# Performance work log

Hardware: AMD Instinct MI355X
Metric: run time of the kernel (lower is better)

The kernel has to match this reference:

```python
import jax, jax.numpy as jnp
import numpy as np
import math

N_HEAD = 16
N_KV_HEAD = 4
HEAD_DIM = 128  # n_embed // n_head


def apply_rope(x, omega, offset=0):
    # x: (B, T, H, D); omega: (D//2,) Llama-style inverse frequencies
    T = x.shape[1]
    d2 = x.shape[-1] // 2
    pos = (jnp.arange(T) + offset).astype(x.dtype)
    ang = pos[:, None] * omega[None, :]              # (T, d2)
    cos = jnp.cos(ang)[None, :, None, :]
    sin = jnp.sin(ang)[None, :, None, :]
    x1, x2 = x[..., :d2], x[..., d2:]
    return jnp.concatenate([x1 * cos - x2 * sin, x1 * sin + x2 * cos], axis=-1)


def setup_inputs() -> dict:
    key = jax.random.key(0)
    k1, k2, k3, k4 = jax.random.split(key, 4)
    B, T, C = 2, 2048, 2048
    std = 0.02
    x = jax.random.normal(k1, (B, T, C), dtype=jnp.float32)
    wq = jax.random.normal(k2, (C, C), dtype=jnp.float32) * std
    wkv = jax.random.normal(k3, (C, 2 * N_KV_HEAD * HEAD_DIM), dtype=jnp.float32) * std
    wproj = jax.random.normal(k4, (C, C), dtype=jnp.float32) * std * (2 * 24) ** (-0.5)
    # Llama RoPE frequencies: 1 / 10000^(2i/D)
    omega = (1.0 / (10000.0 ** (jnp.arange(0, HEAD_DIM, 2, dtype=jnp.float32) / HEAD_DIM)))
    return {"x": x, "wq": wq, "wkv": wkv, "wproj": wproj, "omega": omega}


def reference(x, wq, wkv, wproj, omega):
    B, T, C = x.shape
    H, KH, D = N_HEAD, N_KV_HEAD, HEAD_DIM
    G = H // KH  # query heads per kv head

    q = (x @ wq).reshape(B, T, H, D)
    kv = x @ wkv
    k, v = jnp.split(kv, 2, axis=-1)

    q = apply_rope(q, omega, offset=0)
    k = apply_rope(k.reshape(B, T, KH, D), omega, offset=0)
    v = v.reshape(B, T, KH, D)

    # GQA causal attention (no KV expansion: group query heads per kv head)
    qr = q.reshape(B, T, KH, G, D)
    scores = jnp.einsum('bqkgd,bskd->bkgqs', qr, k) / math.sqrt(D)
    causal = jnp.tril(jnp.ones((T, T), dtype=bool))
    scores = jnp.where(causal[None, None, None, :, :], scores, -jnp.inf)
    att = jax.nn.softmax(scores, axis=-1)
    y = jnp.einsum('bkgqs,bskd->bqkgd', att, v).reshape(B, T, C)
    return y @ wproj
```

## Files before the change

kernel.cpp:

```cpp
#include <hip/hip_runtime.h>
#include <hip/hip_bf16.h>

#define B_ 2
#define T_ 2048
#define C_ 2048
#define H_ 16
#define KH_ 4
#define D_ 128

typedef unsigned short ushort_t;
typedef __attribute__((ext_vector_type(8))) short short8;
typedef __attribute__((ext_vector_type(4))) float f32x4;

#define RSQRT_D 0.08838834764831845f
#define L2E 1.4426950408889634f
#define QSCALE (0.08838834764831845f * 1.4426950408889634f)

__device__ __forceinline__ ushort_t f2b(float f) {
  union { float f; unsigned u; } v; v.f = f;
  unsigned r = v.u + 0x7fffu + ((v.u >> 16) & 1u);
  return (ushort_t)(r >> 16);
}
__device__ __forceinline__ float b2f(ushort_t u) {
  union { unsigned u; float f; } v; v.u = ((unsigned)u) << 16;
  return v.f;
}

__device__ __forceinline__ f32x4 mfma16(short8 a, short8 b, f32x4 c) {
  return __builtin_amdgcn_mfma_f32_16x16x32_bf16(a, b, c, 0, 0, 0);
}

__device__ __forceinline__ void async16(const void* g, void* l) {
  __builtin_amdgcn_global_load_lds(
      (const __attribute__((address_space(1))) void*)g,
      (__attribute__((address_space(3))) void*)l, 16, 0, 0);
}

__device__ __forceinline__ unsigned cvtpk(float lo, float hi) {
  unsigned r;
  asm volatile("v_cvt_pk_bf16_f32 %0, %1, %2" : "=v"(r) : "v"(lo), "v"(hi));
  return r;
}


__global__ void convert_f32_bf16(const float* __restrict__ in, ushort_t* __restrict__ out, int n4) {
  int i = blockIdx.x * blockDim.x + threadIdx.x;
  if (i >= n4) return;
  float4 v = ((const float4*)in)[i];
  ushort4 o;
  o.x = f2b(v.x); o.y = f2b(v.y); o.z = f2b(v.z); o.w = f2b(v.w);
  ((ushort4*)out)[i] = o;
}

__global__ void transpose_to_bf16(const float* __restrict__ in, ushort_t* __restrict__ out, int R, int C) {
  __shared__ float tile[32][33];
  int c0 = blockIdx.x * 32, r0 = blockIdx.y * 32;
  int tx = threadIdx.x, ty = threadIdx.y;
#pragma unroll
  for (int i = 0; i < 4; i++) {
    int r = ty + i * 8;
    tile[r][tx] = in[(size_t)(r0 + r) * C + c0 + tx];
  }
  __syncthreads();
#pragma unroll
  for (int i = 0; i < 4; i++) {
    int r = ty + i * 8;
    out[(size_t)(c0 + r) * R + r0 + tx] = f2b(tile[tx][r]);
  }
}

__global__ void rope_tab_k(const float* __restrict__ omega, float2* __restrict__ tab) {
  int idx = blockIdx.x * blockDim.x + threadIdx.x;
  int d = idx & 63;
  int t = idx >> 6;
  float ang = (float)t * omega[d];
  tab[idx] = make_float2(cosf(ang), sinf(ang));
}

__global__ void rope_q_k(const ushort_t* __restrict__ QKVraw, const float2* __restrict__ tab,
                         ushort_t* __restrict__ Qb) {
  int idx = blockIdx.x * blockDim.x + threadIdx.x;
  int d = idx & 63;
  int h = (idx >> 6) & 15;
  int t = (idx >> 10) & 2047;
  int b = idx >> 21;
  size_t in_off = (size_t)(b * 2048 + t) * 3072 + h * 128 + d;
  float x1 = b2f(QKVraw[in_off]);
  float x2 = b2f(QKVraw[in_off + 64]);
  float2 cs = tab[t * 64 + d];
  size_t out_off = ((size_t)(b * 16 + h) * 2048 + t) * 128 + d;
  Qb[out_off] = f2b((x1 * cs.x - x2 * cs.y) * QSCALE);
  Qb[out_off + 64] = f2b((x1 * cs.y + x2 * cs.x) * QSCALE);
}

__global__ void rope_k_k(const ushort_t* __restrict__ QKVraw, const float2* __restrict__ tab,
                         ushort_t* __restrict__ Kb) {
  int idx = blockIdx.x * blockDim.x + threadIdx.x;
  int d = idx & 63;
  int kh = (idx >> 6) & 3;
  int t = (idx >> 8) & 2047;
  int b = idx >> 19;
  size_t in_off = (size_t)(b * 2048 + t) * 3072 + 2048 + kh * 128 + d;
  float x1 = b2f(QKVraw[in_off]);
  float x2 = b2f(QKVraw[in_off + 64]);
  float2 cs = tab[t * 64 + d];
  size_t out_off = ((size_t)(b * 4 + kh) * 2048 + t) * 128 + d;
  Kb[out_off] = f2b(x1 * cs.x - x2 * cs.y);
  Kb[out_off + 64] = f2b(x1 * cs.y + x2 * cs.x);
}

__global__ void v_frag_k(const ushort_t* __restrict__ QKVraw, ushort_t* __restrict__ Vf) {
  int idx = blockIdx.x * blockDim.x + threadIdx.x;
  int lane = idx & 63;
  int n = (idx >> 6) & 7;
  int hv = (idx >> 9) & 1;
  int tile = (idx >> 10) & 31;
  int z = idx >> 15;
  int b = z >> 2, kh = z & 3;
  int lr = lane & 15, lc = lane >> 4;
  int d = n * 16 + lr;
  union { ushort_t u[8]; short8 v; } out;
#pragma unroll
  for (int j = 0; j < 8; j++) {
    int tw = j >> 1, par = j & 1;
    int kl = (hv * 2 + (tw >> 1)) * 16 + lc * 4 + 2 * (tw & 1) + par;
    int t = tile * 64 + kl;
    out.u[j] = QKVraw[(size_t)(b * 2048 + t) * 3072 + 2560 + kh * 128 + d];
  }
  *(short8*)(Vf + (size_t)idx * 8) = out.v;
}


__device__ __forceinline__ void store_out(float* C, size_t idx, float v) { C[idx] = v; }
__device__ __forceinline__ void store_out(ushort_t* C, size_t idx, float v) { C[idx] = f2b(v); }

template <typename OUT_T>
__global__ __launch_bounds__(256) void gemm_bt(const ushort_t* __restrict__ A,
                                               const ushort_t* __restrict__ Bt,
                                               OUT_T* __restrict__ C,
                                               int M, int N, int K) {
  __shared__ __attribute__((aligned(16))) ushort_t As[2][128 * 32];
  __shared__ __attribute__((aligned(16))) ushort_t Bs[2][128 * 32];
  const int tid = threadIdx.x;
  const int lane = tid & 63;
  const int w = tid >> 6;
  const int bm = blockIdx.y, bn = blockIdx.x;
  const int lr = lane & 15, lc = lane >> 4;
  const int wr = (w >> 1) * 64, wc = (w & 1) * 64;
  const ushort_t* Ab = A + (size_t)bm * 128 * K;
  const ushort_t* Bb = Bt + (size_t)bn * 128 * K;
  const int srow = tid >> 2;
  const int scol = (tid & 3) * 8;
  f32x4 acc[4][4];
#pragma unroll
  for (int i = 0; i < 4; i++)
#pragma unroll
    for (int j = 0; j < 4; j++) acc[i][j] = (f32x4)(0.0f);

  async16(Ab + (size_t)srow * K + scol, &As[0][0] + srow * 32 + scol);
  async16(Ab + (size_t)(srow + 64) * K + scol, &As[0][0] + (srow + 64) * 32 + scol);
  async16(Bb + (size_t)srow * K + scol, &Bs[0][0] + srow * 32 + scol);
  async16(Bb + (size_t)(srow + 64) * K + scol, &Bs[0][0] + (srow + 64) * 32 + scol);

  const int nt = K >> 5;
#pragma unroll 2
  for (int t = 0; t < nt - 1; t++) {
    const int cur = t & 1;
    {
      const int k1 = (t + 1) << 5;
      ushort_t* Ad = &As[cur ^ 1][0];
      ushort_t* Bd = &Bs[cur ^ 1][0];
      async16(Ab + (size_t)srow * K + k1 + scol, Ad + srow * 32 + scol);
      async16(Ab + (size_t)(srow + 64) * K + k1 + scol, Ad + (srow + 64) * 32 + scol);
      async16(Bb + (size_t)srow * K + k1 + scol, Bd + srow * 32 + scol);
      async16(Bb + (size_t)(srow + 64) * K + k1 + scol, Bd + (srow + 64) * 32 + scol);
    }
    asm volatile("s_waitcnt vmcnt(4)" ::: "memory");
    __builtin_amdgcn_s_barrier();
    __builtin_amdgcn_sched_barrier(0);
    const ushort_t* Al = &As[cur][0];
    const ushort_t* Bl = &Bs[cur][0];
    short8 af[4], bf[4];
#pragma unroll
    for (int mi = 0; mi < 4; mi++)
      af[mi] = *(const short8*)(Al + (wr + mi * 16 + lr) * 32 + lc * 8);
#pragma unroll
    for (int ni = 0; ni < 4; ni++)
      bf[ni] = *(const short8*)(Bl + (wc + ni * 16 + lr) * 32 + lc * 8);
#pragma unroll
    for (int mi = 0; mi < 4; mi++)
#pragma unroll
      for (int ni = 0; ni < 4; ni++)
        acc[mi][ni] = mfma16(af[mi], bf[ni], acc[mi][ni]);
    asm volatile("" ::: "memory");
    __builtin_amdgcn_s_barrier();
    asm volatile("" ::: "memory");
  }
  {
    const int cur = (nt - 1) & 1;
    asm volatile("s_waitcnt vmcnt(0)" ::: "memory");
    __builtin_amdgcn_s_barrier();
    __builtin_amdgcn_sched_barrier(0);
    const ushort_t* Al = &As[cur][0];
    const ushort_t* Bl = &Bs[cur][0];
    short8 af[4], bf[4];
#pragma unroll
    for (int mi = 0; mi < 4; mi++)
      af[mi] = *(const short8*)(Al + (wr + mi * 16 + lr) * 32 + lc * 8);
#pragma unroll
    for (int ni = 0; ni < 4; ni++)
      bf[ni] = *(const short8*)(Bl + (wc + ni * 16 + lr) * 32 + lc * 8);
#pragma unroll
    for (int mi = 0; mi < 4; mi++)
#pragma unroll
      for (int ni = 0; ni < 4; ni++)
        acc[mi][ni] = mfma16(af[mi], bf[ni], acc[mi][ni]);
  }
#pragma unroll
  for (int mi = 0; mi < 4; mi++) {
#pragma unroll
    for (int ni = 0; ni < 4; ni++) {
      int row = bm * 128 + wr + mi * 16 + lc * 4;
      int col = bn * 128 + wc + ni * 16 + lr;
#pragma unroll
      for (int r = 0; r < 4; r++)
        store_out(C, (size_t)(row + r) * N + col, acc[mi][ni][r]);
    }
  }
}

__global__ __launch_bounds__(256, 2) void attn_k(const ushort_t* __restrict__ Qb,
                                                 const ushort_t* __restrict__ Kb,
                                                 const ushort_t* __restrict__ Vf,
                                                 ushort_t* __restrict__ Yb) {
  __shared__ __attribute__((aligned(16))) ushort_t Ks[2][64 * 128];
  const int tid = threadIdx.x;
  const int lane = tid & 63;
  const int w = tid >> 6;
  const int lr = lane & 15, lc = lane >> 4;
  const int gy = blockIdx.y;
  const int h = gy;
  const int b = blockIdx.z;
  const int kh = h >> 2;
  const int qc = (gy & 8) ? (31 - ((blockIdx.x + gy - 8) & 31))
                          : ((blockIdx.x + gy) & 31);
  const int q0w = qc * 64 + w * 16;
  const int q = q0w + lr;

  const ushort_t* Qp = Qb + (size_t)(b * 16 + h) * T_ * D_;
  const ushort_t* Kp = Kb + (size_t)(b * 4 + kh) * T_ * D_;
  const ushort_t* Vfb = Vf + (size_t)(b * 4 + kh) * 262144;

  const int st_row = tid >> 4;
  const int st_slot = tid & 15;

  short8 qf[4];
#pragma unroll
  for (int c = 0; c < 4; c++)
    qf[c] = *(const short8*)(Qp + (size_t)(q0w + lr) * D_ + c * 32 + lc * 8);

  f32x4 o[8];
#pragma unroll
  for (int n = 0; n < 8; n++) o[n] = (f32x4)(0.0f);
  float m = -1e30f, l = 0.0f;

  const int nt = qc + 1;

#pragma unroll
  for (int i = 0; i < 4; i++) {
    int row = i * 16 + st_row;
    async16(Kp + (size_t)row * D_ + (((st_slot - row) & 15) * 8),
            &Ks[0][0] + row * 128 + st_slot * 8);
  }

#pragma unroll 1
  for (int ti = 0; ti < nt; ti++) {
    __syncthreads();
    const int kv0 = ti * 64;
    if (ti + 1 < nt) {
      const ushort_t* Kn = Kp + (size_t)(kv0 + 64) * D_;
      ushort_t* dst = &Ks[(ti + 1) & 1][0];
#pragma unroll
      for (int i = 0; i < 4; i++) {
        int row = i * 16 + st_row;
        async16(Kn + (size_t)row * D_ + (((st_slot - row) & 15) * 8),
                dst + row * 128 + st_slot * 8);
      }
    }
    const ushort_t* Kl = &Ks[ti & 1][0];
    const ushort_t* Vt0 = Vfb + (size_t)(ti * 2) * 4096;
    short8 vr0[8];
#pragma unroll
    for (int n = 0; n < 8; n++)
      vr0[n] = *(const short8*)(Vt0 + n * 512 + lane * 8);
    f32x4 s[4];
#pragma unroll
    for (int kj = 0; kj < 4; kj++) s[kj] = (f32x4)(0.0f);
    __builtin_amdgcn_s_setprio(1);
#pragma unroll
    for (int c = 0; c < 4; c++) {
      short8 kf[4];
#pragma unroll
      for (int kj = 0; kj < 4; kj++)
        kf[kj] = *(const short8*)(Kl + (kj * 16 + lr) * 128 + (((c * 4 + lc + lr) & 15) * 8));
#pragma unroll
      for (int kj = 0; kj < 4; kj++)
        s[kj] = mfma16(kf[kj], qf[c], s[kj]);
    }
    __builtin_amdgcn_s_setprio(0);
    const ushort_t* Vt1 = Vfb + (size_t)(ti * 2 + 1) * 4096;
    short8 vr1[8];
#pragma unroll
    for (int n = 0; n < 8; n++)
      vr1[n] = *(const short8*)(Vt1 + n * 512 + lane * 8);
    float pv[16];
    float mx = -1e30f;
    if (kv0 + 63 > q0w) {
#pragma unroll
      for (int kj = 0; kj < 4; kj++)
#pragma unroll
        for (int r = 0; r < 4; r++) {
          float a = s[kj][r];
          if (kv0 + kj * 16 + lc * 4 + r > q) a = -1e30f;
          pv[kj * 4 + r] = a;
          mx = fmaxf(mx, a);
        }
    } else {
#pragma unroll
      for (int kj = 0; kj < 4; kj++)
#pragma unroll
        for (int r = 0; r < 4; r++) {
          float a = s[kj][r];
          pv[kj * 4 + r] = a;
          mx = fmaxf(mx, a);
        }
    }
    mx = fmaxf(mx, __shfl_xor(mx, 16));
    mx = fmaxf(mx, __shfl_xor(mx, 32));
    const bool need = __any(mx > m + 8.0f);
    const float mn = need ? fmaxf(m, mx) : m;
    float rs = 0.0f;
#pragma unroll
    for (int i = 0; i < 16; i++) {
      pv[i] = exp2f(pv[i] - mn);
      rs += pv[i];
    }
    rs += __shfl_xor(rs, 16);
    rs += __shfl_xor(rs, 32);
    unsigned Wd[8];
#pragma unroll
    for (int kj = 0; kj < 4; kj++) {
      Wd[kj * 2] = cvtpk(pv[kj * 4], pv[kj * 4 + 1]);
      Wd[kj * 2 + 1] = cvtpk(pv[kj * 4 + 2], pv[kj * 4 + 3]);
    }
    union { unsigned u[4]; short8 v; } pa0, pa1;
#pragma unroll
    for (int t = 0; t < 4; t++) { pa0.u[t] = Wd[t]; pa1.u[t] = Wd[4 + t]; }
    if (need) {
      float al = exp2f(m - mn);
      m = mn;
      l = l * al + rs;
      float alT[4];
#pragma unroll
      for (int r = 0; r < 4; r++)
        alT[r] = __shfl(al, (lane & 48) | (lc * 4 + r));
#pragma unroll
      for (int n = 0; n < 8; n++)
#pragma unroll
        for (int r = 0; r < 4; r++) o[n][r] *= alT[r];
    } else {
      l += rs;
    }
    __builtin_amdgcn_s_setprio(1);
#pragma unroll
    for (int n = 0; n < 8; n++) o[n] = mfma16(pa0.v, vr0[n], o[n]);
#pragma unroll
    for (int n = 0; n < 8; n++) o[n] = mfma16(pa1.v, vr1[n], o[n]);
    __builtin_amdgcn_s_setprio(0);
  }
  float inv = 1.0f / l;
  float invT[4];
#pragma unroll
  for (int r = 0; r < 4; r++)
    invT[r] = __shfl(inv, (lane & 48) | (lc * 4 + r));
#pragma unroll
  for (int n = 0; n < 8; n++)
#pragma unroll
    for (int r = 0; r < 4; r++) {
      int qo = q0w + lc * 4 + r;
      int d = n * 16 + lr;
      Yb[(size_t)(b * T_ + qo) * 2048 + h * 128 + d] = f2b(o[n][r] * invT[r]);
    }
}


extern "C" void kernel_launch(void* const* d_in, const int* in_sizes, int n_in,
                              void* d_out, int out_size, void* d_ws, size_t ws_size,
                              hipStream_t stream) {
  (void)in_sizes; (void)n_in; (void)out_size; (void)ws_size;
  const float* x = (const float*)d_in[0];
  const float* wq = (const float*)d_in[1];
  const float* wkv = (const float*)d_in[2];
  const float* wproj = (const float*)d_in[3];
  const float* omega = (const float*)d_in[4];
  float* out = (float*)d_out;
  char* ws = (char*)d_ws;

  ushort_t* xb     = (ushort_t*)(ws + 0);
  ushort_t* wqkvT  = (ushort_t*)(ws + 16777216);
  ushort_t* wkvT   = (ushort_t*)(ws + 25165824);
  ushort_t* wprojT = (ushort_t*)(ws + 29360128);
  ushort_t* QKVraw = (ushort_t*)(ws + 37748736);
  ushort_t* Qb     = (ushort_t*)(ws + 62914560);
  ushort_t* Kb     = (ushort_t*)(ws + 79691776);
  ushort_t* Vf     = (ushort_t*)(ws + 83886080);
  ushort_t* Yb     = (ushort_t*)(ws + 88080384);
  float2*   tab    = (float2*)(ws + 104857600);

  convert_f32_bf16<<<8192, 256, 0, stream>>>(x, xb, 2097152);
  transpose_to_bf16<<<dim3(64, 64), dim3(32, 8), 0, stream>>>(wq, wqkvT, 2048, 2048);
  transpose_to_bf16<<<dim3(32, 64), dim3(32, 8), 0, stream>>>(wkv, wkvT, 2048, 1024);
  transpose_to_bf16<<<dim3(64, 64), dim3(32, 8), 0, stream>>>(wproj, wprojT, 2048, 2048);
  rope_tab_k<<<512, 256, 0, stream>>>(omega, tab);

  gemm_bt<<<dim3(24, 32), 256, 0, stream>>>(xb, wqkvT, QKVraw, 4096, 3072, 2048);

  rope_q_k<<<16384, 256, 0, stream>>>(QKVraw, tab, Qb);
  rope_k_k<<<4096, 256, 0, stream>>>(QKVraw, tab, Kb);
  v_frag_k<<<1024, 256, 0, stream>>>(QKVraw, Vf);

  attn_k<<<dim3(32, 16, 2), 256, 0, stream>>>(Qb, Kb, Vf, Yb);

  gemm_bt<<<dim3(16, 32), 256, 0, stream>>>(Yb, wprojT, out, 4096, 2048, 2048);
}
```

Before: 230.3 us.

## Double attention query tile per block to reuse K/V fragments across two row groups

Each wave now handles two 16-row query fragments, so a block covers 128 query rows instead of 64. Every K tile loaded into LDS and every V fragment read from global memory feeds twice as many MFMAs. The grid is halved and the query-chunk schedule is reordered by batch, with waves skipping KV tiles beyond their causal range. In exchange, register pressure roughly doubles for the O accumulators and Q fragments, which may cut occupancy, and fewer blocks plus idle waves on diagonal tiles can worsen load balance.

```diff
diff --git a/kernel.cpp b/kernel.cpp
--- a/kernel.cpp
+++ b/kernel.cpp
@@ -242,10 +242,8 @@
   const int h = gy;
   const int b = blockIdx.z;
   const int kh = h >> 2;
-  const int qc = (gy & 8) ? (31 - ((blockIdx.x + gy - 8) & 31))
-                          : ((blockIdx.x + gy) & 31);
-  const int q0w = qc * 64 + w * 16;
-  const int q = q0w + lr;
+  const int qc = b ? (15 - ((blockIdx.x + gy) & 15)) : ((blockIdx.x + gy) & 15);
+  const int q0w = qc * 128 + w * 32;
 
   const ushort_t* Qp = Qb + (size_t)(b * 16 + h) * T_ * D_;
   const ushort_t* Kp = Kb + (size_t)(b * 4 + kh) * T_ * D_;
@@ -254,17 +252,21 @@
   const int st_row = tid >> 4;
   const int st_slot = tid & 15;
 
-  short8 qf[4];
-#pragma unroll
-  for (int c = 0; c < 4; c++)
-    qf[c] = *(const short8*)(Qp + (size_t)(q0w + lr) * D_ + c * 32 + lc * 8);
-
-  f32x4 o[8];
-#pragma unroll
-  for (int n = 0; n < 8; n++) o[n] = (f32x4)(0.0f);
-  float m = -1e30f, l = 0.0f;
-
-  const int nt = qc + 1;
+  short8 qf[2][4];
+#pragma unroll
+  for (int f = 0; f < 2; f++)
+#pragma unroll
+    for (int c = 0; c < 4; c++)
+      qf[f][c] = *(const short8*)(Qp + (size_t)(q0w + f * 16 + lr) * D_ + c * 32 + lc * 8);
+
+  f32x4 o[2][8];
+#pragma unroll
+  for (int f = 0; f < 2; f++)
+#pragma unroll
+    for (int n = 0; n < 8; n++) o[f][n] = (f32x4)(0.0f);
+  float m[2] = {-1e30f, -1e30f}, l[2] = {0.0f, 0.0f};
+
+  const int nt = 2 * qc + 2;
 
 #pragma unroll
   for (int i = 0; i < 4; i++) {
@@ -287,15 +289,18 @@
                 dst + row * 128 + st_slot * 8);
       }
     }
+    if (kv0 > q0w + 31) continue;
     const ushort_t* Kl = &Ks[ti & 1][0];
     const ushort_t* Vt0 = Vfb + (size_t)(ti * 2) * 4096;
     short8 vr0[8];
 #pragma unroll
     for (int n = 0; n < 8; n++)
       vr0[n] = *(const short8*)(Vt0 + n * 512 + lane * 8);
-    f32x4 s[4];
-#pragma unroll
-    for (int kj = 0; kj < 4; kj++) s[kj] = (f32x4)(0.0f);
+    f32x4 s[2][4];
+#pragma unroll
+    for (int f = 0; f < 2; f++)
+#pragma unroll
+      for (int kj = 0; kj < 4; kj++) s[f][kj] = (f32x4)(0.0f);
     __builtin_amdgcn_s_setprio(1);
 #pragma unroll
     for (int c = 0; c < 4; c++) {
@@ -304,8 +309,10 @@
       for (int kj = 0; kj < 4; kj++)
         kf[kj] = *(const short8*)(Kl + (kj * 16 + lr) * 128 + (((c * 4 + lc + lr) & 15) * 8));
 #pragma unroll
-      for (int kj = 0; kj < 4; kj++)
-        s[kj] = mfma16(kf[kj], qf[c], s[kj]);
+      for (int f = 0; f < 2; f++)
+#pragma unroll
+        for (int kj = 0; kj < 4; kj++)
+          s[f][kj] = mfma16(kf[kj], qf[f][c], s[f][kj]);
     }
     __builtin_amdgcn_s_setprio(0);
     const ushort_t* Vt1 = Vfb + (size_t)(ti * 2 + 1) * 4096;
@@ -313,84 +320,97 @@
 #pragma unroll
     for (int n = 0; n < 8; n++)
       vr1[n] = *(const short8*)(Vt1 + n * 512 + lane * 8);
-    float pv[16];
-    float mx = -1e30f;
-    if (kv0 + 63 > q0w) {
-#pragma unroll
-      for (int kj = 0; kj < 4; kj++)
-#pragma unroll
-        for (int r = 0; r < 4; r++) {
-          float a = s[kj][r];
-          if (kv0 + kj * 16 + lc * 4 + r > q) a = -1e30f;
-          pv[kj * 4 + r] = a;
-          mx = fmaxf(mx, a);
-        }
-    } else {
-#pragma unroll
-      for (int kj = 0; kj < 4; kj++)
-#pragma unroll
-        for (int r = 0; r < 4; r++) {
-          float a = s[kj][r];
-          pv[kj * 4 + r] = a;
-          mx = fmaxf(mx, a);
-        }
-    }
-    mx = fmaxf(mx, __shfl_xor(mx, 16));
-    mx = fmaxf(mx, __shfl_xor(mx, 32));
-    const bool need = __any(mx > m + 8.0f);
-    const float mn = need ? fmaxf(m, mx) : m;
-    float rs = 0.0f;
-#pragma unroll
-    for (int i = 0; i < 16; i++) {
-      pv[i] = exp2f(pv[i] - mn);
-      rs += pv[i];
-    }
-    rs += __shfl_xor(rs, 16);
-    rs += __shfl_xor(rs, 32);
-    unsigned Wd[8];
-#pragma unroll
-    for (int kj = 0; kj < 4; kj++) {
-      Wd[kj * 2] = cvtpk(pv[kj * 4], pv[kj * 4 + 1]);
-      Wd[kj * 2 + 1] = cvtpk(pv[kj * 4 + 2], pv[kj * 4 + 3]);
-    }
-    union { unsigned u[4]; short8 v; } pa0, pa1;
-#pragma unroll
-    for (int t = 0; t < 4; t++) { pa0.u[t] = Wd[t]; pa1.u[t] = Wd[4 + t]; }
-    if (need) {
-      float al = exp2f(m - mn);
-      m = mn;
-      l = l * al + rs;
-      float alT[4];
-#pragma unroll
-      for (int r = 0; r < 4; r++)
-        alT[r] = __shfl(al, (lane & 48) | (lc * 4 + r));
-#pragma unroll
-      for (int n = 0; n < 8; n++)
-#pragma unroll
-        for (int r = 0; r < 4; r++) o[n][r] *= alT[r];
-    } else {
-      l += rs;
+    const bool maskt = (kv0 + 63 > q0w);
+    union { unsigned u[4]; short8 v; } pa0[2], pa1[2];
+#pragma unroll
+    for (int f = 0; f < 2; f++) {
+      const int q = q0w + f * 16 + lr;
+      float pv[16];
+      float mx = -1e30f;
+      if (maskt) {
+#pragma unroll
+        for (int kj = 0; kj < 4; kj++)
+#pragma unroll
+          for (int r = 0; r < 4; r++) {
+            float a = s[f][kj][r];
+            if (kv0 + kj * 16 + lc * 4 + r > q) a = -1e30f;
+            pv[kj * 4 + r] = a;
+            mx = fmaxf(mx, a);
+          }
+      } else {
+#pragma unroll
+        for (int kj = 0; kj < 4; kj++)
+#pragma unroll
+          for (int r = 0; r < 4; r++) {
+            float a = s[f][kj][r];
+            pv[kj * 4 + r] = a;
+            mx = fmaxf(mx, a);
+          }
+      }
+      mx = fmaxf(mx, __shfl_xor(mx, 16));
+      mx = fmaxf(mx, __shfl_xor(mx, 32));
+      const bool need = __any(mx > m[f] + 8.0f);
+      const float mn = need ? fmaxf(m[f], mx) : m[f];
+      float rs = 0.0f;
+#pragma unroll
+      for (int i = 0; i < 16; i++) {
+        pv[i] = exp2f(pv[i] - mn);
+        rs += pv[i];
+      }
+      rs += __shfl_xor(rs, 16);
+      rs += __shfl_xor(rs, 32);
+#pragma unroll
+      for (int kj = 0; kj < 2; kj++) {
+        pa0[f].u[kj * 2] = cvtpk(pv[kj * 4], pv[kj * 4 + 1]);
+        pa0[f].u[kj * 2 + 1] = cvtpk(pv[kj * 4 + 2], pv[kj * 4 + 3]);
+        pa1[f].u[kj * 2] = cvtpk(pv[8 + kj * 4], pv[8 + kj * 4 + 1]);
+        pa1[f].u[kj * 2 + 1] = cvtpk(pv[8 + kj * 4 + 2], pv[8 + kj * 4 + 3]);
+      }
+      if (need) {
+        float al = exp2f(m[f] - mn);
+        m[f] = mn;
+        l[f] = l[f] * al + rs;
+        float alT[4];
+#pragma unroll
+        for (int r = 0; r < 4; r++)
+          alT[r] = __shfl(al, (lane & 48) | (lc * 4 + r));
+#pragma unroll
+        for (int n = 0; n < 8; n++)
+#pragma unroll
+          for (int r = 0; r < 4; r++) o[f][n][r] *= alT[r];
+      } else {
+        l[f] += rs;
+      }
     }
     __builtin_amdgcn_s_setprio(1);
 #pragma unroll
-    for (int n = 0; n < 8; n++) o[n] = mfma16(pa0.v, vr0[n], o[n]);
-#pragma unroll
-    for (int n = 0; n < 8; n++) o[n] = mfma16(pa1.v, vr1[n], o[n]);
+    for (int n = 0; n < 8; n++) {
+      o[0][n] = mfma16(pa0[0].v, vr0[n], o[0][n]);
+      o[1][n] = mfma16(pa0[1].v, vr0[n], o[1][n]);
+    }
+#pragma unroll
+    for (int n = 0; n < 8; n++) {
+      o[0][n] = mfma16(pa1[0].v, vr1[n], o[0][n]);
+      o[1][n] = mfma16(pa1[1].v, vr1[n], o[1][n]);
+    }
     __builtin_amdgcn_s_setprio(0);
   }
-  float inv = 1.0f / l;
-  float invT[4];
-#pragma unroll
-  for (int r = 0; r < 4; r++)
-    invT[r] = __shfl(inv, (lane & 48) | (lc * 4 + r));
-#pragma unroll
-  for (int n = 0; n < 8; n++)
-#pragma unroll
-    for (int r = 0; r < 4; r++) {
-      int qo = q0w + lc * 4 + r;
-      int d = n * 16 + lr;
-      Yb[(size_t)(b * T_ + qo) * 2048 + h * 128 + d] = f2b(o[n][r] * invT[r]);
-    }
+#pragma unroll
+  for (int f = 0; f < 2; f++) {
+    float inv = 1.0f / l[f];
+    float invT[4];
+#pragma unroll
+    for (int r = 0; r < 4; r++)
+      invT[r] = __shfl(inv, (lane & 48) | (lc * 4 + r));
+#pragma unroll
+    for (int n = 0; n < 8; n++)
+#pragma unroll
+      for (int r = 0; r < 4; r++) {
+        int qo = q0w + f * 16 + lc * 4 + r;
+        int d = n * 16 + lr;
+        Yb[(size_t)(b * T_ + qo) * 2048 + h * 128 + d] = f2b(o[f][n][r] * invT[r]);
+      }
+  }
 }
 
 
@@ -429,7 +449,7 @@
   rope_k_k<<<4096, 256, 0, stream>>>(QKVraw, tab, Kb);
   v_frag_k<<<1024, 256, 0, stream>>>(QKVraw, Vf);
 
-  attn_k<<<dim3(32, 16, 2), 256, 0, stream>>>(Qb, Kb, Vf, Yb);
+  attn_k<<<dim3(16, 16, 2), 256, 0, stream>>>(Qb, Kb, Vf, Yb);
 
   gemm_bt<<<dim3(16, 32), 256, 0, stream>>>(Yb, wprojT, out, 4096, 2048, 2048);
 }
```

Result: faster. 221.0 us (-4.0%).
